# Kernel optimization log

Hardware: AMD Instinct MI355X
Metric: run time of the kernel (lower is better)

The kernel has to match this reference:

```python
import jax, jax.numpy as jnp
import numpy as np
import math

EMBED_DIM = 768
NUM_HEADS = 12
HEAD_DIM = EMBED_DIM // NUM_HEADS
B, T = 4, 2048
GATE_EPS = 1e-06


def setup_inputs() -> dict:
    key = jax.random.key(0)
    ks = jax.random.split(key, 10)
    s_in = 1.0 / math.sqrt(EMBED_DIM)   # fan-in init scale for D->hd projections
    s_hd = 1.0 / math.sqrt(HEAD_DIM)    # fan-in init scale for hd->D projection
    return {
        "hidden_states": jax.random.normal(ks[0], (B, T, EMBED_DIM), dtype=jnp.float32),
        "Wq": jax.random.normal(ks[1], (NUM_HEADS, EMBED_DIM, HEAD_DIM), dtype=jnp.float32) * s_in,
        "bq": jax.random.normal(ks[2], (NUM_HEADS, HEAD_DIM), dtype=jnp.float32) * s_in,
        "Wk": jax.random.normal(ks[3], (NUM_HEADS, EMBED_DIM, HEAD_DIM), dtype=jnp.float32) * s_in,
        "bk": jax.random.normal(ks[4], (NUM_HEADS, HEAD_DIM), dtype=jnp.float32) * s_in,
        "Wv": jax.random.normal(ks[5], (NUM_HEADS, EMBED_DIM, HEAD_DIM), dtype=jnp.float32) * s_in,
        "bv": jax.random.normal(ks[6], (NUM_HEADS, HEAD_DIM), dtype=jnp.float32) * s_in,
        "Wo": jax.random.normal(ks[7], (NUM_HEADS, HEAD_DIM, EMBED_DIM), dtype=jnp.float32) * s_hd,
        "bo": jax.random.normal(ks[8], (NUM_HEADS, EMBED_DIM), dtype=jnp.float32) * s_hd,
        "gate": jnp.ones((NUM_HEADS,), dtype=jnp.float32),
    }


def reference(hidden_states, Wq, bq, Wk, bk, Wv, bv, Wo, bo, gate):
    # Batched per-head QKV projections: btd,hde->bhte
    Q = jnp.einsum("btd,hde->bhte", hidden_states, Wq) + bq[None, :, None, :]
    K = jnp.einsum("btd,hde->bhte", hidden_states, Wk) + bk[None, :, None, :]
    V = jnp.einsum("btd,hde->bhte", hidden_states, Wv) + bv[None, :, None, :]
    scores = jnp.einsum("bhqe,bhke->bhqk", Q, K) / math.sqrt(HEAD_DIM)  # [B,H,T,T]
    weights = jax.nn.softmax(scores, axis=-1)
    attn = jnp.einsum("bhqk,bhke->bhqe", weights, V)  # [B,H,T,hd]
    # Per-head output projection (bias included), gated; zero out heads with gate < eps
    per_head = jnp.einsum("bhte,hed->bhtd", attn, Wo) + bo[None, :, None, :]
    g = jnp.where(gate < GATE_EPS, 0.0, gate)  # replicate host-side skip as mask
    out = jnp.einsum("bhtd,h->btd", per_head, g)  # gated sum over heads
    return out
```

## Files before the change

### kernel.cpp

```cpp
#include <hip/hip_runtime.h>
#include <math.h>

#define NH 12
#define DM 768
#define HD 64
#define BB 4
#define TT 2048
#define MTOT (BB*TT)

#define QSCALE 0.1803368801111204f

typedef short bf16x8 __attribute__((ext_vector_type(8)));
typedef float f32x4 __attribute__((ext_vector_type(4)));
typedef int   i32x4 __attribute__((ext_vector_type(4)));
typedef unsigned int u32;

#define GLDS(g, l) __builtin_amdgcn_global_load_lds((const __attribute__((address_space(1))) u32*)(g), (__attribute__((address_space(3))) u32*)(l), 16, 0, 0)

__device__ __forceinline__ unsigned short f2bf(float f) {
    unsigned u = __float_as_uint(f);
    u += 0x7fff + ((u >> 16) & 1);
    return (unsigned short)(u >> 16);
}

__global__ void k_pack_x(const float* __restrict__ x, unsigned short* __restrict__ xb) {
    int i = (blockIdx.x * blockDim.x + threadIdx.x) * 4;
    float4 v = *(const float4*)(x + i);
    ushort4 o = { f2bf(v.x), f2bf(v.y), f2bf(v.z), f2bf(v.w) };
    *(ushort4*)(xb + i) = o;
}

__global__ void k_pack_wqkv(const float* __restrict__ Wq, const float* __restrict__ Wk,
                            const float* __restrict__ Wv, unsigned short* __restrict__ wt) {
    __shared__ unsigned short L[64][72];
    const int bid = blockIdx.x;
    const int q = bid / 144, r = bid % 144, h = r / 12, kt = r % 12;
    const float* W = (q == 0 ? Wq : (q == 1 ? Wk : Wv)) + (size_t)h * DM * HD + (size_t)kt * 64 * HD;
    #pragma unroll
    for (int it = 0; it < 4; it++) {
        int idx = it * 256 + threadIdx.x;
        int rr = idx >> 4, e4 = (idx & 15) * 4;
        float4 v = *(const float4*)&W[(size_t)rr * HD + e4];
        L[e4    ][rr] = f2bf(v.x);
        L[e4 + 1][rr] = f2bf(v.y);
        L[e4 + 2][rr] = f2bf(v.z);
        L[e4 + 3][rr] = f2bf(v.w);
    }
    __syncthreads();
    #pragma unroll
    for (int it = 0; it < 2; it++) {
        int idx = it * 256 + threadIdx.x;
        int e = idx >> 3, c8 = (idx & 7) * 8;
        *(bf16x8*)&wt[(size_t)(q * 768 + h * 64 + e) * DM + kt * 64 + c8] = *(const bf16x8*)&L[e][c8];
    }
}

__global__ void k_pack_wo(const float* __restrict__ Wo, const float* __restrict__ gate,
                          unsigned short* __restrict__ wt) {
    __shared__ unsigned short L[64][72];
    const int bid = blockIdx.x;
    const int ht = bid / 12, dt = bid % 12;
    float g = gate[ht]; g = (g < 1e-6f) ? 0.f : g;
    const float* W = Wo + (size_t)ht * 64 * DM + dt * 64;
    #pragma unroll
    for (int it = 0; it < 4; it++) {
        int idx = it * 256 + threadIdx.x;
        int rr = idx >> 4, d4 = (idx & 15) * 4;
        float4 v = *(const float4*)&W[(size_t)rr * DM + d4];
        L[d4    ][rr] = f2bf(g * v.x);
        L[d4 + 1][rr] = f2bf(g * v.y);
        L[d4 + 2][rr] = f2bf(g * v.z);
        L[d4 + 3][rr] = f2bf(g * v.w);
    }
    __syncthreads();
    #pragma unroll
    for (int it = 0; it < 2; it++) {
        int idx = it * 256 + threadIdx.x;
        int d = idx >> 3, c8 = (idx & 7) * 8;
        *(bf16x8*)&wt[(size_t)(dt * 64 + d) * DM + ht * 64 + c8] = *(const bf16x8*)&L[d][c8];
    }
}

__global__ void k_bias_o(const float* __restrict__ bo, const float* __restrict__ gate,
                         float* __restrict__ bias) {
    int d = blockIdx.x * blockDim.x + threadIdx.x;
    if (d < DM) {
        float s = 0.f;
        #pragma unroll
        for (int h = 0; h < NH; h++) {
            float g = gate[h]; g = (g < 1e-6f) ? 0.f : g;
            s += g * bo[h * DM + d];
        }
        bias[d] = s;
    }
}

__global__ __launch_bounds__(256) void k_gemm_qkv(
    const unsigned short* __restrict__ A,
    const unsigned short* __restrict__ Bt,
    const float* __restrict__ bq, const float* __restrict__ bk, const float* __restrict__ bv,
    unsigned short* __restrict__ Q, unsigned short* __restrict__ Kg, unsigned short* __restrict__ Vt)
{
    __shared__ unsigned short As[2][4096];
    __shared__ unsigned short Bs[2][4096];
    const int m0 = blockIdx.y * 128, n0 = blockIdx.x * 128;
    const int tid = threadIdx.x, lane = tid & 63, w = tid >> 6;
    const int wr = (w >> 1) * 64, wc = (w & 1) * 64;
    const int lr = lane & 15, lq = lane >> 4;

    const int arow = tid >> 2;
    const int ag   = ((tid & 3) ^ (arow & 3)) * 8;
    const int ldsw = w * 512;
    const int kg = (lq ^ (lr & 3)) * 8;

    #define STAGE_G(k0_, buf_) do { \
        const unsigned short* a_ = A  + (size_t)(m0 + arow) * DM + (k0_) + ag; \
        const unsigned short* b_ = Bt + (size_t)(n0 + arow) * DM + (k0_) + ag; \
        GLDS(a_,             &As[buf_][ldsw]); \
        GLDS(a_ + 64 * DM,   &As[buf_][2048 + ldsw]); \
        GLDS(b_,             &Bs[buf_][ldsw]); \
        GLDS(b_ + 64 * DM,   &Bs[buf_][2048 + ldsw]); \
    } while (0)

    f32x4 acc[4][4] = {};
    STAGE_G(0, 0);
    for (int it = 0; it < DM / 32; it++) {
        const int cur = it & 1;
        __syncthreads();
        if (it < DM / 32 - 1) STAGE_G((it + 1) * 32, cur ^ 1);
        bf16x8 af[4], bf[4];
        #pragma unroll
        for (int rt = 0; rt < 4; rt++) af[rt] = *(const bf16x8*)&As[cur][(wr + rt*16 + lr) * 32 + kg];
        #pragma unroll
        for (int ct = 0; ct < 4; ct++) bf[ct] = *(const bf16x8*)&Bs[cur][(wc + ct*16 + lr) * 32 + kg];
        #pragma unroll
        for (int rt = 0; rt < 4; rt++)
            #pragma unroll
            for (int ct = 0; ct < 4; ct++)
                acc[rt][ct] = __builtin_amdgcn_mfma_f32_16x16x32_bf16(af[rt], bf[ct], acc[rt][ct], 0, 0, 0);
    }
    #undef STAGE_G

    const int region = n0 / DM;
    const int b  = m0 >> 11;
    const int tb = m0 & 2047;
    if (region == 2) {
        #pragma unroll
        for (int rt = 0; rt < 4; rt++)
          #pragma unroll
          for (int ct = 0; ct < 4; ct++) {
            int n = n0 + wc + ct*16 + lr, r = n - 2*DM;
            int h = r >> 6, e = r & 63;
            int t0 = tb + wr + rt*16 + lq*4;
            float bias = bv[r];
            ushort4 o;
            o.x = f2bf(acc[rt][ct][0] + bias);
            o.y = f2bf(acc[rt][ct][1] + bias);
            o.z = f2bf(acc[rt][ct][2] + bias);
            o.w = f2bf(acc[rt][ct][3] + bias);
            *(ushort4*)&Vt[((size_t)(b*NH + h)*HD + e)*TT + t0] = o;
          }
    } else {
        const float* bias_p = (region == 0) ? bq : bk;
        const float  scale  = (region == 0) ? QSCALE : 1.0f;
        unsigned short* dst = (region == 0) ? Q : Kg;
        #pragma unroll
        for (int rt = 0; rt < 4; rt++)
          #pragma unroll
          for (int ct = 0; ct < 4; ct++) {
            int n = n0 + wc + ct*16 + lr, r = n - region*DM;
            int h = r >> 6, e = r & 63;
            float bias = bias_p[r];
            #pragma unroll
            for (int i = 0; i < 4; i++) {
                int t = tb + wr + rt*16 + lq*4 + i;
                dst[((size_t)(b*NH + h)*TT + t)*HD + e] = f2bf((acc[rt][ct][i] + bias) * scale);
            }
          }
    }
}

__global__ __launch_bounds__(256) void k_flash(
    const unsigned short* __restrict__ Q, const unsigned short* __restrict__ Kg,
    const unsigned short* __restrict__ Vt, unsigned short* __restrict__ A2)
{
    __shared__ unsigned short Ks[2][4096];
    __shared__ unsigned short Vs[2][4096];
    const int bh = blockIdx.x, qt = blockIdx.y;
    const int b = bh / NH, h = bh % NH;
    const int tid = threadIdx.x, lane = tid & 63, w = tid >> 6;
    const int col = lane & 15, quad = lane >> 4;
    const size_t qk_base = (size_t)bh * TT * HD;
    const size_t vt_base = (size_t)bh * HD * TT;
    const int tq0 = qt * 128 + w * 32;

    const int srow  = tid >> 3;
    const int sperm = (tid & 7) ^ (srow & 7);
    const int koff0 = srow * HD + sperm * 8;
    const int voff0 = srow * TT + sperm * 8;
    const int lds0  = w * 512;

    const unsigned short* ksrc = Kg + qk_base;
    const unsigned short* vsrc = Vt + vt_base;

    const int c7 = col & 7;
    const int ra0 = col * 64 + (((    quad) ^ c7) * 8);
    const int ra1 = col * 64 + (((4 + quad) ^ c7) * 8);

    bf16x8 aq[2][2];
    #pragma unroll
    for (int rt = 0; rt < 2; rt++)
        #pragma unroll
        for (int ks = 0; ks < 2; ks++)
            aq[rt][ks] = *(const bf16x8*)&Q[qk_base + (size_t)(tq0 + rt*16 + col) * HD + ks*32 + quad*8];

    f32x4 co[4][2] = {};
    float l_part[2] = { 0.f, 0.f };

    const int srcA = (((quad * 2    ) & 3) << 4) | col;
    const int srcB = (((quad * 2 + 1) & 3) << 4) | col;

    #define STAGE(kt_, buf_) do { \
        const unsigned short* kb_ = ksrc + (size_t)(kt_) * 64 * HD; \
        const unsigned short* vb_ = vsrc + (kt_) * 64; \
        GLDS(kb_ + koff0,           &Ks[buf_][lds0]); \
        GLDS(kb_ + koff0 + 32*HD,   &Ks[buf_][lds0 + 2048]); \
        GLDS(vb_ + voff0,           &Vs[buf_][lds0]); \
        GLDS(vb_ + voff0 + 32*TT,   &Vs[buf_][lds0 + 2048]); \
    } while (0)

    STAGE(0, 0);

    for (int kt = 0; kt < TT/64; kt++) {
        const int cur = kt & 1;
        __syncthreads();
        if (kt < TT/64 - 1) STAGE(kt + 1, cur ^ 1);

        bf16x8 kf[4][2];
        #pragma unroll
        for (int ct = 0; ct < 4; ct++) {
            kf[ct][0] = *(const bf16x8*)&Ks[cur][ct*1024 + ra0];
            kf[ct][1] = *(const bf16x8*)&Ks[cur][ct*1024 + ra1];
        }

        f32x4 cs[4][2] = {};
        #pragma unroll
        for (int ks = 0; ks < 2; ks++)
            #pragma unroll
            for (int ct = 0; ct < 4; ct++)
                #pragma unroll
                for (int rt = 0; rt < 2; rt++)
                    cs[ct][rt] = __builtin_amdgcn_mfma_f32_16x16x32_bf16(kf[ct][ks], aq[rt][ks], cs[ct][rt], 0, 0, 0);

        int pk[2][4][2];
        #pragma unroll
        for (int rt = 0; rt < 2; rt++) {
            float ps[4][4];
            float ssum = 0.f;
            #pragma unroll
            for (int ct = 0; ct < 4; ct++)
                #pragma unroll
                for (int i = 0; i < 4; i++) {
                    float p = __builtin_amdgcn_exp2f(cs[ct][rt][i]);
                    ps[ct][i] = p;
                    ssum += p;
                }
            l_part[rt] += ssum;
            #pragma unroll
            for (int ct = 0; ct < 4; ct++) {
                pk[rt][ct][0] = (int)__builtin_amdgcn_perm(__float_as_uint(ps[ct][1]), __float_as_uint(ps[ct][0]), 0x07060302u);
                pk[rt][ct][1] = (int)__builtin_amdgcn_perm(__float_as_uint(ps[ct][3]), __float_as_uint(ps[ct][2]), 0x07060302u);
            }
        }

        #pragma unroll
        for (int k4 = 0; k4 < 2; k4++) {
            bf16x8 pt[2];
            #pragma unroll
            for (int rt = 0; rt < 2; rt++) {
                int a0 = __shfl(pk[rt][2*k4  ][0], srcA);
                int b0 = __shfl(pk[rt][2*k4+1][0], srcA);
                int a1 = __shfl(pk[rt][2*k4  ][1], srcA);
                int b1 = __shfl(pk[rt][2*k4+1][1], srcA);
                int a2 = __shfl(pk[rt][2*k4  ][0], srcB);
                int b2 = __shfl(pk[rt][2*k4+1][0], srcB);
                int a3 = __shfl(pk[rt][2*k4  ][1], srcB);
                int b3 = __shfl(pk[rt][2*k4+1][1], srcB);
                i32x4 di;
                di[0] = (quad < 2) ? a0 : b0;
                di[1] = (quad < 2) ? a1 : b1;
                di[2] = (quad < 2) ? a2 : b2;
                di[3] = (quad < 2) ? a3 : b3;
                pt[rt] = __builtin_bit_cast(bf16x8, di);
            }
            const int rav = (k4 == 0) ? ra0 : ra1;
            #pragma unroll
            for (int cv = 0; cv < 4; cv++) {
                bf16x8 vf = *(const bf16x8*)&Vs[cur][cv*1024 + rav];
                #pragma unroll
                for (int rt = 0; rt < 2; rt++)
                    co[cv][rt] = __builtin_amdgcn_mfma_f32_16x16x32_bf16(vf, pt[rt], co[cv][rt], 0, 0, 0);
            }
        }
    }
    #undef STAGE

    #pragma unroll
    for (int rt = 0; rt < 2; rt++) {
        float l = l_part[rt];
        l += __shfl_xor(l, 16);
        l += __shfl_xor(l, 32);
        float inv = 1.0f / l;
        int t = tq0 + rt*16 + col;
        #pragma unroll
        for (int cv = 0; cv < 4; cv++) {
            ushort4 o;
            o.x = f2bf(co[cv][rt][0] * inv);
            o.y = f2bf(co[cv][rt][1] * inv);
            o.z = f2bf(co[cv][rt][2] * inv);
            o.w = f2bf(co[cv][rt][3] * inv);
            *(ushort4*)&A2[(size_t)(b*TT + t) * DM + h*HD + cv*16 + quad*4] = o;
        }
    }
}

__global__ __launch_bounds__(256) void k_gemm_out(
    const unsigned short* __restrict__ A,
    const unsigned short* __restrict__ Bt,
    const float* __restrict__ bias,
    float* __restrict__ out)
{
    __shared__ unsigned short As[2][4096];
    __shared__ unsigned short Bs[2][4096];
    const int m0 = blockIdx.y * 128, n0 = blockIdx.x * 128;
    const int tid = threadIdx.x, lane = tid & 63, w = tid >> 6;
    const int wr = (w >> 1) * 64, wc = (w & 1) * 64;
    const int lr = lane & 15, lq = lane >> 4;

    const int arow = tid >> 2;
    const int ag   = ((tid & 3) ^ (arow & 3)) * 8;
    const int ldsw = w * 512;
    const int kg = (lq ^ (lr & 3)) * 8;

    #define STAGE_G(k0_, buf_) do { \
        const unsigned short* a_ = A  + (size_t)(m0 + arow) * DM + (k0_) + ag; \
        const unsigned short* b_ = Bt + (size_t)(n0 + arow) * DM + (k0_) + ag; \
        GLDS(a_,             &As[buf_][ldsw]); \
        GLDS(a_ + 64 * DM,   &As[buf_][2048 + ldsw]); \
        GLDS(b_,             &Bs[buf_][ldsw]); \
        GLDS(b_ + 64 * DM,   &Bs[buf_][2048 + ldsw]); \
    } while (0)

    f32x4 acc[4][4] = {};
    STAGE_G(0, 0);
    for (int it = 0; it < DM / 32; it++) {
        const int cur = it & 1;
        __syncthreads();
        if (it < DM / 32 - 1) STAGE_G((it + 1) * 32, cur ^ 1);
        bf16x8 af[4], bf[4];
        #pragma unroll
        for (int rt = 0; rt < 4; rt++) af[rt] = *(const bf16x8*)&As[cur][(wr + rt*16 + lr) * 32 + kg];
        #pragma unroll
        for (int ct = 0; ct < 4; ct++) bf[ct] = *(const bf16x8*)&Bs[cur][(wc + ct*16 + lr) * 32 + kg];
        #pragma unroll
        for (int rt = 0; rt < 4; rt++)
            #pragma unroll
            for (int ct = 0; ct < 4; ct++)
                acc[rt][ct] = __builtin_amdgcn_mfma_f32_16x16x32_bf16(af[rt], bf[ct], acc[rt][ct], 0, 0, 0);
    }
    #undef STAGE_G

    #pragma unroll
    for (int rt = 0; rt < 4; rt++)
      #pragma unroll
      for (int ct = 0; ct < 4; ct++)
        #pragma unroll
        for (int i = 0; i < 4; i++) {
            int m = m0 + wr + rt*16 + lq*4 + i;
            int n = n0 + wc + ct*16 + lr;
            out[(size_t)m * DM + n] = acc[rt][ct][i] + bias[n];
        }
}

extern "C" void kernel_launch(void* const* d_in, const int* in_sizes, int n_in,
                              void* d_out, int out_size, void* d_ws, size_t ws_size,
                              hipStream_t stream) {
    const float* x    = (const float*)d_in[0];
    const float* Wq   = (const float*)d_in[1];
    const float* bq   = (const float*)d_in[2];
    const float* Wk   = (const float*)d_in[3];
    const float* bk   = (const float*)d_in[4];
    const float* Wv   = (const float*)d_in[5];
    const float* bv   = (const float*)d_in[6];
    const float* Wo   = (const float*)d_in[7];
    const float* bo   = (const float*)d_in[8];
    const float* gate = (const float*)d_in[9];
    float* out = (float*)d_out;

    char* p = (char*)d_ws;
    unsigned short* Xb   = (unsigned short*)p;  p += (size_t)MTOT*DM*2;
    unsigned short* Wqkv = (unsigned short*)p;  p += (size_t)3*DM*DM*2;
    unsigned short* Qb   = (unsigned short*)p;  p += (size_t)BB*NH*TT*HD*2;
    unsigned short* Kb   = (unsigned short*)p;  p += (size_t)BB*NH*TT*HD*2;
    unsigned short* Vtb  = (unsigned short*)p;  p += (size_t)BB*NH*TT*HD*2;
    unsigned short* A2   = (unsigned short*)p;  p += (size_t)MTOT*DM*2;
    unsigned short* Wob  = (unsigned short*)p;  p += (size_t)DM*DM*2;
    float*          bio  = (float*)p;           p += (size_t)DM*4;

    k_pack_x   <<<(MTOT*DM/4 + 255)/256, 256, 0, stream>>>(x, Xb);
    k_pack_wqkv<<<3*12*12, 256, 0, stream>>>(Wq, Wk, Wv, Wqkv);
    k_pack_wo  <<<12*12, 256, 0, stream>>>(Wo, gate, Wob);
    k_bias_o   <<<3, 256, 0, stream>>>(bo, gate, bio);
    k_gemm_qkv <<<dim3((3*DM)/128, MTOT/128), 256, 0, stream>>>(Xb, Wqkv, bq, bk, bv, Qb, Kb, Vtb);
    k_flash    <<<dim3(BB*NH, TT/128), 256, 0, stream>>>(Qb, Kb, Vtb, A2);
    k_gemm_out <<<dim3(DM/128, MTOT/128), 256, 0, stream>>>(A2, Wob, bio, out);
}
```

Measured before the change: 279.2 us.

## Merge prep kernels into one launch and shrink flash tiles to 64 queries

The four packing and bias kernels become one k_prep launch that picks its job from the block index, which removes three kernel launches. The flash attention kernel now gives each wave 16 query rows instead of 32 and steps through 32-key tiles instead of 64, halving LDS use and doubling the grid to 1536 blocks for better occupancy. In exchange, each K/V tile loaded into LDS is reused by fewer queries, so global K/V traffic doubles and twice as many loop iterations and barriers run. The softmax still uses exp2 with no running max, as before.

```diff
diff --git a/kernel.cpp b/kernel.cpp
--- a/kernel.cpp
+++ b/kernel.cpp
@@ -23,75 +23,74 @@
     return (unsigned short)(u >> 16);
 }
 
-__global__ void k_pack_x(const float* __restrict__ x, unsigned short* __restrict__ xb) {
-    int i = (blockIdx.x * blockDim.x + threadIdx.x) * 4;
-    float4 v = *(const float4*)(x + i);
-    ushort4 o = { f2bf(v.x), f2bf(v.y), f2bf(v.z), f2bf(v.w) };
-    *(ushort4*)(xb + i) = o;
-}
-
-__global__ void k_pack_wqkv(const float* __restrict__ Wq, const float* __restrict__ Wk,
-                            const float* __restrict__ Wv, unsigned short* __restrict__ wt) {
+__global__ void k_prep(const float* __restrict__ x,
+                       const float* __restrict__ Wq, const float* __restrict__ Wk,
+                       const float* __restrict__ Wv, const float* __restrict__ Wo,
+                       const float* __restrict__ bo, const float* __restrict__ gate,
+                       unsigned short* __restrict__ xb, unsigned short* __restrict__ wqkv,
+                       unsigned short* __restrict__ wob, float* __restrict__ bio)
+{
     __shared__ unsigned short L[64][72];
     const int bid = blockIdx.x;
-    const int q = bid / 144, r = bid % 144, h = r / 12, kt = r % 12;
-    const float* W = (q == 0 ? Wq : (q == 1 ? Wk : Wv)) + (size_t)h * DM * HD + (size_t)kt * 64 * HD;
-    #pragma unroll
-    for (int it = 0; it < 4; it++) {
-        int idx = it * 256 + threadIdx.x;
-        int rr = idx >> 4, e4 = (idx & 15) * 4;
-        float4 v = *(const float4*)&W[(size_t)rr * HD + e4];
-        L[e4    ][rr] = f2bf(v.x);
-        L[e4 + 1][rr] = f2bf(v.y);
-        L[e4 + 2][rr] = f2bf(v.z);
-        L[e4 + 3][rr] = f2bf(v.w);
-    }
-    __syncthreads();
-    #pragma unroll
-    for (int it = 0; it < 2; it++) {
-        int idx = it * 256 + threadIdx.x;
-        int e = idx >> 3, c8 = (idx & 7) * 8;
-        *(bf16x8*)&wt[(size_t)(q * 768 + h * 64 + e) * DM + kt * 64 + c8] = *(const bf16x8*)&L[e][c8];
-    }
-}
-
-__global__ void k_pack_wo(const float* __restrict__ Wo, const float* __restrict__ gate,
-                          unsigned short* __restrict__ wt) {
-    __shared__ unsigned short L[64][72];
-    const int bid = blockIdx.x;
-    const int ht = bid / 12, dt = bid % 12;
-    float g = gate[ht]; g = (g < 1e-6f) ? 0.f : g;
-    const float* W = Wo + (size_t)ht * 64 * DM + dt * 64;
-    #pragma unroll
-    for (int it = 0; it < 4; it++) {
-        int idx = it * 256 + threadIdx.x;
-        int rr = idx >> 4, d4 = (idx & 15) * 4;
-        float4 v = *(const float4*)&W[(size_t)rr * DM + d4];
-        L[d4    ][rr] = f2bf(g * v.x);
-        L[d4 + 1][rr] = f2bf(g * v.y);
-        L[d4 + 2][rr] = f2bf(g * v.z);
-        L[d4 + 3][rr] = f2bf(g * v.w);
-    }
-    __syncthreads();
-    #pragma unroll
-    for (int it = 0; it < 2; it++) {
-        int idx = it * 256 + threadIdx.x;
-        int d = idx >> 3, c8 = (idx & 7) * 8;
-        *(bf16x8*)&wt[(size_t)(dt * 64 + d) * DM + ht * 64 + c8] = *(const bf16x8*)&L[d][c8];
-    }
-}
-
-__global__ void k_bias_o(const float* __restrict__ bo, const float* __restrict__ gate,
-                         float* __restrict__ bias) {
-    int d = blockIdx.x * blockDim.x + threadIdx.x;
-    if (d < DM) {
-        float s = 0.f;
-        #pragma unroll
-        for (int h = 0; h < NH; h++) {
-            float g = gate[h]; g = (g < 1e-6f) ? 0.f : g;
-            s += g * bo[h * DM + d];
-        }
-        bias[d] = s;
+    if (bid < 6144) {
+        int i = (bid * 256 + threadIdx.x) * 4;
+        float4 v = *(const float4*)(x + i);
+        ushort4 o = { f2bf(v.x), f2bf(v.y), f2bf(v.z), f2bf(v.w) };
+        *(ushort4*)(xb + i) = o;
+    } else if (bid < 6576) {
+        int b2 = bid - 6144;
+        int q = b2 / 144, r = b2 % 144, h = r / 12, kt = r % 12;
+        const float* W = (q == 0 ? Wq : (q == 1 ? Wk : Wv)) + (size_t)h * DM * HD + (size_t)kt * 64 * HD;
+        #pragma unroll
+        for (int it = 0; it < 4; it++) {
+            int idx = it * 256 + threadIdx.x;
+            int rr = idx >> 4, e4 = (idx & 15) * 4;
+            float4 v = *(const float4*)&W[(size_t)rr * HD + e4];
+            L[e4    ][rr] = f2bf(v.x);
+            L[e4 + 1][rr] = f2bf(v.y);
+            L[e4 + 2][rr] = f2bf(v.z);
+            L[e4 + 3][rr] = f2bf(v.w);
+        }
+        __syncthreads();
+        #pragma unroll
+        for (int it = 0; it < 2; it++) {
+            int idx = it * 256 + threadIdx.x;
+            int e = idx >> 3, c8 = (idx & 7) * 8;
+            *(bf16x8*)&wqkv[(size_t)(q * 768 + h * 64 + e) * DM + kt * 64 + c8] = *(const bf16x8*)&L[e][c8];
+        }
+    } else if (bid < 6720) {
+        int b2 = bid - 6576;
+        int ht = b2 / 12, dt = b2 % 12;
+        float g = gate[ht]; g = (g < 1e-6f) ? 0.f : g;
+        const float* W = Wo + (size_t)ht * 64 * DM + dt * 64;
+        #pragma unroll
+        for (int it = 0; it < 4; it++) {
+            int idx = it * 256 + threadIdx.x;
+            int rr = idx >> 4, d4 = (idx & 15) * 4;
+            float4 v = *(const float4*)&W[(size_t)rr * DM + d4];
+            L[d4    ][rr] = f2bf(g * v.x);
+            L[d4 + 1][rr] = f2bf(g * v.y);
+            L[d4 + 2][rr] = f2bf(g * v.z);
+            L[d4 + 3][rr] = f2bf(g * v.w);
+        }
+        __syncthreads();
+        #pragma unroll
+        for (int it = 0; it < 2; it++) {
+            int idx = it * 256 + threadIdx.x;
+            int d = idx >> 3, c8 = (idx & 7) * 8;
+            *(bf16x8*)&wob[(size_t)(dt * 64 + d) * DM + ht * 64 + c8] = *(const bf16x8*)&L[d][c8];
+        }
+    } else {
+        int d = (bid - 6720) * 256 + threadIdx.x;
+        if (d < DM) {
+            float s = 0.f;
+            #pragma unroll
+            for (int h = 0; h < NH; h++) {
+                float g = gate[h]; g = (g < 1e-6f) ? 0.f : g;
+                s += g * bo[h * DM + d];
+            }
+            bio[d] = s;
+        }
     }
 }
 
@@ -184,143 +183,110 @@
     const unsigned short* __restrict__ Q, const unsigned short* __restrict__ Kg,
     const unsigned short* __restrict__ Vt, unsigned short* __restrict__ A2)
 {
-    __shared__ unsigned short Ks[2][4096];
-    __shared__ unsigned short Vs[2][4096];
+    __shared__ unsigned short Ks[2][2048];
+    __shared__ unsigned short Vs[2][2048];
     const int bh = blockIdx.x, qt = blockIdx.y;
     const int b = bh / NH, h = bh % NH;
     const int tid = threadIdx.x, lane = tid & 63, w = tid >> 6;
     const int col = lane & 15, quad = lane >> 4;
     const size_t qk_base = (size_t)bh * TT * HD;
     const size_t vt_base = (size_t)bh * HD * TT;
-    const int tq0 = qt * 128 + w * 32;
-
-    const int srow  = tid >> 3;
-    const int sperm = (tid & 7) ^ (srow & 7);
-    const int koff0 = srow * HD + sperm * 8;
-    const int voff0 = srow * TT + sperm * 8;
-    const int lds0  = w * 512;
+    const int tq0 = qt * 64 + w * 16;
+
+    const int krow = tid >> 3;
+    const int koff = krow * HD + (((tid & 7) ^ (krow & 7)) * 8);
+    const int ve   = tid >> 2;
+    const int voff = ve * TT + (((tid & 3) ^ (ve & 3)) * 8);
+    const int lds0 = w * 512;
 
     const unsigned short* ksrc = Kg + qk_base;
     const unsigned short* vsrc = Vt + vt_base;
 
     const int c7 = col & 7;
-    const int ra0 = col * 64 + (((    quad) ^ c7) * 8);
-    const int ra1 = col * 64 + (((4 + quad) ^ c7) * 8);
-
-    bf16x8 aq[2][2];
+    const int kr0 = col * 64 + ((quad       ^ c7) * 8);
+    const int kr1 = col * 64 + (((4 + quad) ^ c7) * 8);
+    const int vr  = col * 32 + ((quad ^ (col & 3)) * 8);
+
+    bf16x8 aq[2];
+    aq[0] = *(const bf16x8*)&Q[qk_base + (size_t)(tq0 + col) * HD +      quad*8];
+    aq[1] = *(const bf16x8*)&Q[qk_base + (size_t)(tq0 + col) * HD + 32 + quad*8];
+
+    f32x4 co[4] = {};
+    float l_part = 0.f;
+
+    const int srcA = (((quad & 1) * 2    ) << 4) | col;
+    const int srcB = (((quad & 1) * 2 + 1) << 4) | col;
+
+    #define STAGE(kt_, buf_) do { \
+        GLDS(ksrc + (size_t)(kt_) * 32 * HD + koff, &Ks[buf_][lds0]); \
+        GLDS(vsrc + (kt_) * 32 + voff,              &Vs[buf_][lds0]); \
+    } while (0)
+
+    STAGE(0, 0);
+
+    for (int kt = 0; kt < TT/32; kt++) {
+        const int cur = kt & 1;
+        __syncthreads();
+        if (kt < TT/32 - 1) STAGE(kt + 1, cur ^ 1);
+
+        bf16x8 kf00 = *(const bf16x8*)&Ks[cur][kr0];
+        bf16x8 kf01 = *(const bf16x8*)&Ks[cur][kr1];
+        bf16x8 kf10 = *(const bf16x8*)&Ks[cur][1024 + kr0];
+        bf16x8 kf11 = *(const bf16x8*)&Ks[cur][1024 + kr1];
+
+        f32x4 cs0 = {}, cs1 = {};
+        cs0 = __builtin_amdgcn_mfma_f32_16x16x32_bf16(kf00, aq[0], cs0, 0, 0, 0);
+        cs1 = __builtin_amdgcn_mfma_f32_16x16x32_bf16(kf10, aq[0], cs1, 0, 0, 0);
+        cs0 = __builtin_amdgcn_mfma_f32_16x16x32_bf16(kf01, aq[1], cs0, 0, 0, 0);
+        cs1 = __builtin_amdgcn_mfma_f32_16x16x32_bf16(kf11, aq[1], cs1, 0, 0, 0);
+
+        float p00 = __builtin_amdgcn_exp2f(cs0[0]);
+        float p01 = __builtin_amdgcn_exp2f(cs0[1]);
+        float p02 = __builtin_amdgcn_exp2f(cs0[2]);
+        float p03 = __builtin_amdgcn_exp2f(cs0[3]);
+        float p10 = __builtin_amdgcn_exp2f(cs1[0]);
+        float p11 = __builtin_amdgcn_exp2f(cs1[1]);
+        float p12 = __builtin_amdgcn_exp2f(cs1[2]);
+        float p13 = __builtin_amdgcn_exp2f(cs1[3]);
+        l_part += ((p00 + p01) + (p02 + p03)) + ((p10 + p11) + (p12 + p13));
+        int pk00 = (int)__builtin_amdgcn_perm(__float_as_uint(p01), __float_as_uint(p00), 0x07060302u);
+        int pk01 = (int)__builtin_amdgcn_perm(__float_as_uint(p03), __float_as_uint(p02), 0x07060302u);
+        int pk10 = (int)__builtin_amdgcn_perm(__float_as_uint(p11), __float_as_uint(p10), 0x07060302u);
+        int pk11 = (int)__builtin_amdgcn_perm(__float_as_uint(p13), __float_as_uint(p12), 0x07060302u);
+
+        int a00 = __shfl(pk00, srcA), a01 = __shfl(pk01, srcA);
+        int a10 = __shfl(pk10, srcA), a11 = __shfl(pk11, srcA);
+        int b00 = __shfl(pk00, srcB), b01 = __shfl(pk01, srcB);
+        int b10 = __shfl(pk10, srcB), b11 = __shfl(pk11, srcB);
+        bool lo = (quad < 2);
+        i32x4 di;
+        di[0] = lo ? a00 : a10;
+        di[1] = lo ? a01 : a11;
+        di[2] = lo ? b00 : b10;
+        di[3] = lo ? b01 : b11;
+        bf16x8 pt = __builtin_bit_cast(bf16x8, di);
+
+        #pragma unroll
+        for (int cv = 0; cv < 4; cv++) {
+            bf16x8 vf = *(const bf16x8*)&Vs[cur][cv*512 + vr];
+            co[cv] = __builtin_amdgcn_mfma_f32_16x16x32_bf16(vf, pt, co[cv], 0, 0, 0);
+        }
+    }
+    #undef STAGE
+
+    float l = l_part;
+    l += __shfl_xor(l, 16);
+    l += __shfl_xor(l, 32);
+    float inv = 1.0f / l;
+    int t = tq0 + col;
     #pragma unroll
-    for (int rt = 0; rt < 2; rt++)
-        #pragma unroll
-        for (int ks = 0; ks < 2; ks++)
-            aq[rt][ks] = *(const bf16x8*)&Q[qk_base + (size_t)(tq0 + rt*16 + col) * HD + ks*32 + quad*8];
-
-    f32x4 co[4][2] = {};
-    float l_part[2] = { 0.f, 0.f };
-
-    const int srcA = (((quad * 2    ) & 3) << 4) | col;
-    const int srcB = (((quad * 2 + 1) & 3) << 4) | col;
-
-    #define STAGE(kt_, buf_) do { \
-        const unsigned short* kb_ = ksrc + (size_t)(kt_) * 64 * HD; \
-        const unsigned short* vb_ = vsrc + (kt_) * 64; \
-        GLDS(kb_ + koff0,           &Ks[buf_][lds0]); \
-        GLDS(kb_ + koff0 + 32*HD,   &Ks[buf_][lds0 + 2048]); \
-        GLDS(vb_ + voff0,           &Vs[buf_][lds0]); \
-        GLDS(vb_ + voff0 + 32*TT,   &Vs[buf_][lds0 + 2048]); \
-    } while (0)
-
-    STAGE(0, 0);
-
-    for (int kt = 0; kt < TT/64; kt++) {
-        const int cur = kt & 1;
-        __syncthreads();
-        if (kt < TT/64 - 1) STAGE(kt + 1, cur ^ 1);
-
-        bf16x8 kf[4][2];
-        #pragma unroll
-        for (int ct = 0; ct < 4; ct++) {
-            kf[ct][0] = *(const bf16x8*)&Ks[cur][ct*1024 + ra0];
-            kf[ct][1] = *(const bf16x8*)&Ks[cur][ct*1024 + ra1];
-        }
-
-        f32x4 cs[4][2] = {};
-        #pragma unroll
-        for (int ks = 0; ks < 2; ks++)
-            #pragma unroll
-            for (int ct = 0; ct < 4; ct++)
-                #pragma unroll
-                for (int rt = 0; rt < 2; rt++)
-                    cs[ct][rt] = __builtin_amdgcn_mfma_f32_16x16x32_bf16(kf[ct][ks], aq[rt][ks], cs[ct][rt], 0, 0, 0);
-
-        int pk[2][4][2];
-        #pragma unroll
-        for (int rt = 0; rt < 2; rt++) {
-            float ps[4][4];
-            float ssum = 0.f;
-            #pragma unroll
-            for (int ct = 0; ct < 4; ct++)
-                #pragma unroll
-                for (int i = 0; i < 4; i++) {
-                    float p = __builtin_amdgcn_exp2f(cs[ct][rt][i]);
-                    ps[ct][i] = p;
-                    ssum += p;
-                }
-            l_part[rt] += ssum;
-            #pragma unroll
-            for (int ct = 0; ct < 4; ct++) {
-                pk[rt][ct][0] = (int)__builtin_amdgcn_perm(__float_as_uint(ps[ct][1]), __float_as_uint(ps[ct][0]), 0x07060302u);
-                pk[rt][ct][1] = (int)__builtin_amdgcn_perm(__float_as_uint(ps[ct][3]), __float_as_uint(ps[ct][2]), 0x07060302u);
-            }
-        }
-
-        #pragma unroll
-        for (int k4 = 0; k4 < 2; k4++) {
-            bf16x8 pt[2];
-            #pragma unroll
-            for (int rt = 0; rt < 2; rt++) {
-                int a0 = __shfl(pk[rt][2*k4  ][0], srcA);
-                int b0 = __shfl(pk[rt][2*k4+1][0], srcA);
-                int a1 = __shfl(pk[rt][2*k4  ][1], srcA);
-                int b1 = __shfl(pk[rt][2*k4+1][1], srcA);
-                int a2 = __shfl(pk[rt][2*k4  ][0], srcB);
-                int b2 = __shfl(pk[rt][2*k4+1][0], srcB);
-                int a3 = __shfl(pk[rt][2*k4  ][1], srcB);
-                int b3 = __shfl(pk[rt][2*k4+1][1], srcB);
-                i32x4 di;
-                di[0] = (quad < 2) ? a0 : b0;
-                di[1] = (quad < 2) ? a1 : b1;
-                di[2] = (quad < 2) ? a2 : b2;
-                di[3] = (quad < 2) ? a3 : b3;
-                pt[rt] = __builtin_bit_cast(bf16x8, di);
-            }
-            const int rav = (k4 == 0) ? ra0 : ra1;
-            #pragma unroll
-            for (int cv = 0; cv < 4; cv++) {
-                bf16x8 vf = *(const bf16x8*)&Vs[cur][cv*1024 + rav];
-                #pragma unroll
-                for (int rt = 0; rt < 2; rt++)
-                    co[cv][rt] = __builtin_amdgcn_mfma_f32_16x16x32_bf16(vf, pt[rt], co[cv][rt], 0, 0, 0);
-            }
-        }
-    }
-    #undef STAGE
-
-    #pragma unroll
-    for (int rt = 0; rt < 2; rt++) {
-        float l = l_part[rt];
-        l += __shfl_xor(l, 16);
-        l += __shfl_xor(l, 32);
-        float inv = 1.0f / l;
-        int t = tq0 + rt*16 + col;
-        #pragma unroll
-        for (int cv = 0; cv < 4; cv++) {
-            ushort4 o;
-            o.x = f2bf(co[cv][rt][0] * inv);
-            o.y = f2bf(co[cv][rt][1] * inv);
-            o.z = f2bf(co[cv][rt][2] * inv);
-            o.w = f2bf(co[cv][rt][3] * inv);
-            *(ushort4*)&A2[(size_t)(b*TT + t) * DM + h*HD + cv*16 + quad*4] = o;
-        }
+    for (int cv = 0; cv < 4; cv++) {
+        ushort4 o;
+        o.x = f2bf(co[cv][0] * inv);
+        o.y = f2bf(co[cv][1] * inv);
+        o.z = f2bf(co[cv][2] * inv);
+        o.w = f2bf(co[cv][3] * inv);
+        *(ushort4*)&A2[(size_t)(b*TT + t) * DM + h*HD + cv*16 + quad*4] = o;
     }
 }
 
@@ -407,11 +373,8 @@
     unsigned short* Wob  = (unsigned short*)p;  p += (size_t)DM*DM*2;
     float*          bio  = (float*)p;           p += (size_t)DM*4;
 
-    k_pack_x   <<<(MTOT*DM/4 + 255)/256, 256, 0, stream>>>(x, Xb);
-    k_pack_wqkv<<<3*12*12, 256, 0, stream>>>(Wq, Wk, Wv, Wqkv);
-    k_pack_wo  <<<12*12, 256, 0, stream>>>(Wo, gate, Wob);
-    k_bias_o   <<<3, 256, 0, stream>>>(bo, gate, bio);
+    k_prep     <<<6723, 256, 0, stream>>>(x, Wq, Wk, Wv, Wo, bo, gate, Xb, Wqkv, Wob, bio);
     k_gemm_qkv <<<dim3((3*DM)/128, MTOT/128), 256, 0, stream>>>(Xb, Wqkv, bq, bk, bv, Qb, Kb, Vtb);
-    k_flash    <<<dim3(BB*NH, TT/128), 256, 0, stream>>>(Qb, Kb, Vtb, A2);
+    k_flash    <<<dim3(BB*NH, TT/64), 256, 0, stream>>>(Qb, Kb, Vtb, A2);
     k_gemm_out <<<dim3(DM/128, MTOT/128), 256, 0, stream>>>(A2, Wob, bio, out);
 }
```

Result: slower. 285.0 us (+2.0%).

## Merge prep kernels into one launch and triple-buffer K/V in flash attention

Applied to the files above, without the earlier changes.

Folds the four preprocessing kernels (x cast, QKV weight pack, Wo pack, output bias) into a single launch dispatched by block index, which removes three kernel launches. The flash-attention kernel moves from a two-stage to a three-stage K/V LDS ring, prefetching two tiles ahead and using an explicit vmcnt wait plus s_barrier instead of __syncthreads. The deeper prefetch is meant to hide global-load latency better, at the cost of 50% more LDS per block, which may reduce occupancy. The manual waitcnt depends on exactly four outstanding loads per stage being counted correctly.

```diff
diff --git a/kernel.cpp b/kernel.cpp
--- a/kernel.cpp
+++ b/kernel.cpp
@@ -23,75 +23,74 @@
     return (unsigned short)(u >> 16);
 }
 
-__global__ void k_pack_x(const float* __restrict__ x, unsigned short* __restrict__ xb) {
-    int i = (blockIdx.x * blockDim.x + threadIdx.x) * 4;
-    float4 v = *(const float4*)(x + i);
-    ushort4 o = { f2bf(v.x), f2bf(v.y), f2bf(v.z), f2bf(v.w) };
-    *(ushort4*)(xb + i) = o;
-}
-
-__global__ void k_pack_wqkv(const float* __restrict__ Wq, const float* __restrict__ Wk,
-                            const float* __restrict__ Wv, unsigned short* __restrict__ wt) {
+__global__ void k_prep(const float* __restrict__ x,
+                       const float* __restrict__ Wq, const float* __restrict__ Wk,
+                       const float* __restrict__ Wv, const float* __restrict__ Wo,
+                       const float* __restrict__ bo, const float* __restrict__ gate,
+                       unsigned short* __restrict__ xb, unsigned short* __restrict__ wqkv,
+                       unsigned short* __restrict__ wob, float* __restrict__ bio)
+{
     __shared__ unsigned short L[64][72];
     const int bid = blockIdx.x;
-    const int q = bid / 144, r = bid % 144, h = r / 12, kt = r % 12;
-    const float* W = (q == 0 ? Wq : (q == 1 ? Wk : Wv)) + (size_t)h * DM * HD + (size_t)kt * 64 * HD;
-    #pragma unroll
-    for (int it = 0; it < 4; it++) {
-        int idx = it * 256 + threadIdx.x;
-        int rr = idx >> 4, e4 = (idx & 15) * 4;
-        float4 v = *(const float4*)&W[(size_t)rr * HD + e4];
-        L[e4    ][rr] = f2bf(v.x);
-        L[e4 + 1][rr] = f2bf(v.y);
-        L[e4 + 2][rr] = f2bf(v.z);
-        L[e4 + 3][rr] = f2bf(v.w);
-    }
-    __syncthreads();
-    #pragma unroll
-    for (int it = 0; it < 2; it++) {
-        int idx = it * 256 + threadIdx.x;
-        int e = idx >> 3, c8 = (idx & 7) * 8;
-        *(bf16x8*)&wt[(size_t)(q * 768 + h * 64 + e) * DM + kt * 64 + c8] = *(const bf16x8*)&L[e][c8];
-    }
-}
-
-__global__ void k_pack_wo(const float* __restrict__ Wo, const float* __restrict__ gate,
-                          unsigned short* __restrict__ wt) {
-    __shared__ unsigned short L[64][72];
-    const int bid = blockIdx.x;
-    const int ht = bid / 12, dt = bid % 12;
-    float g = gate[ht]; g = (g < 1e-6f) ? 0.f : g;
-    const float* W = Wo + (size_t)ht * 64 * DM + dt * 64;
-    #pragma unroll
-    for (int it = 0; it < 4; it++) {
-        int idx = it * 256 + threadIdx.x;
-        int rr = idx >> 4, d4 = (idx & 15) * 4;
-        float4 v = *(const float4*)&W[(size_t)rr * DM + d4];
-        L[d4    ][rr] = f2bf(g * v.x);
-        L[d4 + 1][rr] = f2bf(g * v.y);
-        L[d4 + 2][rr] = f2bf(g * v.z);
-        L[d4 + 3][rr] = f2bf(g * v.w);
-    }
-    __syncthreads();
-    #pragma unroll
-    for (int it = 0; it < 2; it++) {
-        int idx = it * 256 + threadIdx.x;
-        int d = idx >> 3, c8 = (idx & 7) * 8;
-        *(bf16x8*)&wt[(size_t)(dt * 64 + d) * DM + ht * 64 + c8] = *(const bf16x8*)&L[d][c8];
-    }
-}
-
-__global__ void k_bias_o(const float* __restrict__ bo, const float* __restrict__ gate,
-                         float* __restrict__ bias) {
-    int d = blockIdx.x * blockDim.x + threadIdx.x;
-    if (d < DM) {
-        float s = 0.f;
-        #pragma unroll
-        for (int h = 0; h < NH; h++) {
-            float g = gate[h]; g = (g < 1e-6f) ? 0.f : g;
-            s += g * bo[h * DM + d];
-        }
-        bias[d] = s;
+    if (bid < 6144) {
+        int i = (bid * 256 + threadIdx.x) * 4;
+        float4 v = *(const float4*)(x + i);
+        ushort4 o = { f2bf(v.x), f2bf(v.y), f2bf(v.z), f2bf(v.w) };
+        *(ushort4*)(xb + i) = o;
+    } else if (bid < 6576) {
+        int b2 = bid - 6144;
+        int q = b2 / 144, r = b2 % 144, h = r / 12, kt = r % 12;
+        const float* W = (q == 0 ? Wq : (q == 1 ? Wk : Wv)) + (size_t)h * DM * HD + (size_t)kt * 64 * HD;
+        #pragma unroll
+        for (int it = 0; it < 4; it++) {
+            int idx = it * 256 + threadIdx.x;
+            int rr = idx >> 4, e4 = (idx & 15) * 4;
+            float4 v = *(const float4*)&W[(size_t)rr * HD + e4];
+            L[e4    ][rr] = f2bf(v.x);
+            L[e4 + 1][rr] = f2bf(v.y);
+            L[e4 + 2][rr] = f2bf(v.z);
+            L[e4 + 3][rr] = f2bf(v.w);
+        }
+        __syncthreads();
+        #pragma unroll
+        for (int it = 0; it < 2; it++) {
+            int idx = it * 256 + threadIdx.x;
+            int e = idx >> 3, c8 = (idx & 7) * 8;
+            *(bf16x8*)&wqkv[(size_t)(q * 768 + h * 64 + e) * DM + kt * 64 + c8] = *(const bf16x8*)&L[e][c8];
+        }
+    } else if (bid < 6720) {
+        int b2 = bid - 6576;
+        int ht = b2 / 12, dt = b2 % 12;
+        float g = gate[ht]; g = (g < 1e-6f) ? 0.f : g;
+        const float* W = Wo + (size_t)ht * 64 * DM + dt * 64;
+        #pragma unroll
+        for (int it = 0; it < 4; it++) {
+            int idx = it * 256 + threadIdx.x;
+            int rr = idx >> 4, d4 = (idx & 15) * 4;
+            float4 v = *(const float4*)&W[(size_t)rr * DM + d4];
+            L[d4    ][rr] = f2bf(g * v.x);
+            L[d4 + 1][rr] = f2bf(g * v.y);
+            L[d4 + 2][rr] = f2bf(g * v.z);
+            L[d4 + 3][rr] = f2bf(g * v.w);
+        }
+        __syncthreads();
+        #pragma unroll
+        for (int it = 0; it < 2; it++) {
+            int idx = it * 256 + threadIdx.x;
+            int d = idx >> 3, c8 = (idx & 7) * 8;
+            *(bf16x8*)&wob[(size_t)(dt * 64 + d) * DM + ht * 64 + c8] = *(const bf16x8*)&L[d][c8];
+        }
+    } else {
+        int d = (bid - 6720) * 256 + threadIdx.x;
+        if (d < DM) {
+            float s = 0.f;
+            #pragma unroll
+            for (int h = 0; h < NH; h++) {
+                float g = gate[h]; g = (g < 1e-6f) ? 0.f : g;
+                s += g * bo[h * DM + d];
+            }
+            bio[d] = s;
+        }
     }
 }
 
@@ -184,8 +183,8 @@
     const unsigned short* __restrict__ Q, const unsigned short* __restrict__ Kg,
     const unsigned short* __restrict__ Vt, unsigned short* __restrict__ A2)
 {
-    __shared__ unsigned short Ks[2][4096];
-    __shared__ unsigned short Vs[2][4096];
+    __shared__ unsigned short Ks[3][4096];
+    __shared__ unsigned short Vs[3][4096];
     const int bh = blockIdx.x, qt = blockIdx.y;
     const int b = bh / NH, h = bh % NH;
     const int tid = threadIdx.x, lane = tid & 63, w = tid >> 6;
@@ -230,11 +229,15 @@
     } while (0)
 
     STAGE(0, 0);
-
-    for (int kt = 0; kt < TT/64; kt++) {
-        const int cur = kt & 1;
-        __syncthreads();
-        if (kt < TT/64 - 1) STAGE(kt + 1, cur ^ 1);
+    STAGE(1, 1);
+
+    const int NIT = TT / 64;
+    for (int kt = 0; kt < NIT; kt++) {
+        const int cur = kt % 3;
+        if (kt == NIT - 1) asm volatile("s_waitcnt vmcnt(0)" ::: "memory");
+        else               asm volatile("s_waitcnt vmcnt(4)" ::: "memory");
+        asm volatile("s_barrier" ::: "memory");
+        if (kt < NIT - 2) STAGE(kt + 2, (kt + 2) % 3);
 
         bf16x8 kf[4][2];
         #pragma unroll
@@ -407,10 +410,7 @@
     unsigned short* Wob  = (unsigned short*)p;  p += (size_t)DM*DM*2;
     float*          bio  = (float*)p;           p += (size_t)DM*4;
 
-    k_pack_x   <<<(MTOT*DM/4 + 255)/256, 256, 0, stream>>>(x, Xb);
-    k_pack_wqkv<<<3*12*12, 256, 0, stream>>>(Wq, Wk, Wv, Wqkv);
-    k_pack_wo  <<<12*12, 256, 0, stream>>>(Wo, gate, Wob);
-    k_bias_o   <<<3, 256, 0, stream>>>(bo, gate, bio);
+    k_prep     <<<6723, 256, 0, stream>>>(x, Wq, Wk, Wv, Wo, bo, gate, Xb, Wqkv, Wob, bio);
     k_gemm_qkv <<<dim3((3*DM)/128, MTOT/128), 256, 0, stream>>>(Xb, Wqkv, bq, bk, bv, Qb, Kb, Vtb);
     k_flash    <<<dim3(BB*NH, TT/128), 256, 0, stream>>>(Qb, Kb, Vtb, A2);
     k_gemm_out <<<dim3(DM/128, MTOT/128), 256, 0, stream>>>(A2, Wob, bio, out);
```

Result: slower. 292.5 us (+4.7%).
